# Kernel optimization log

Hardware: AMD Instinct MI355X
Metric: run time of the kernel (lower is better)

The kernel has to match this reference:

```python
import jax, jax.numpy as jnp
import numpy as np

B, S, F, H = 64, 1024, 64, 128


def setup_inputs() -> dict:
    key = jax.random.key(0)
    ks = jax.random.split(key, 12)
    s = 1.0 / np.sqrt(H)
    u = lambda k, shape: jax.random.uniform(k, shape, jnp.float32, -s, s)
    return {
        "x": jax.random.normal(ks[0], (B, S, F), jnp.float32),
        "mu": jax.random.normal(ks[1], (B, 1, F), jnp.float32),
        "W_ih0": u(ks[2], (4 * H, F)),
        "W_hh0": u(ks[3], (4 * H, H)),
        "b_ih0": u(ks[4], (4 * H,)),
        "b_hh0": u(ks[5], (4 * H,)),
        "W_ih1": u(ks[6], (4 * H, H)),
        "W_hh1": u(ks[7], (4 * H, H)),
        "b_ih1": u(ks[8], (4 * H,)),
        "b_hh1": u(ks[9], (4 * H,)),
        "fc_w": u(ks[10], (1, H)),
        "fc_b": u(ks[11], (1,)),
    }


def _cell(x_gates, h, c, Whh, bias):
    # PyTorch LSTM cell: gates ordered i, f, g, o
    g = x_gates + h @ Whh.T + bias
    i, f, gg, o = jnp.split(g, 4, axis=-1)
    c = jax.nn.sigmoid(f) * c + jax.nn.sigmoid(i) * jnp.tanh(gg)
    h = jax.nn.sigmoid(o) * jnp.tanh(c)
    return h, c


def _lstm2(x1, x2, Wih, Whh, bih, bhh):
    # 2-step LSTM layer from zero initial state; returns per-step hidden states
    bias = bih + bhh
    n = x1.shape[0]
    hd = Whh.shape[1]
    h0 = jnp.zeros((n, hd), x1.dtype)
    h1, c1 = _cell(x1 @ Wih.T, h0, h0, Whh, bias)
    h2, _ = _cell(x2 @ Wih.T, h1, c1, Whh, bias)
    return h1, h2


def reference(x, mu, W_ih0, W_hh0, b_ih0, b_hh0, W_ih1, W_hh1, b_ih1, b_hh1, fc_w, fc_b):
    b, s, f = x.shape
    # Every timestep runs an independent 2-step LSTM [x_t, mu] from zero state,
    # so fold (batch, seq) into one big batch of B*S instances.
    x1 = x.reshape(b * s, f)                                   # step-1 inputs
    x2 = jnp.broadcast_to(mu, (b, s, f)).reshape(b * s, f)     # step-2 inputs (mu)
    h1, h2 = _lstm2(x1, x2, W_ih0, W_hh0, b_ih0, b_hh0)        # layer 0
    _, h2 = _lstm2(h1, h2, W_ih1, W_hh1, b_ih1, b_hh1)         # layer 1
    h = jax.nn.relu(h2).reshape(b, s, -1)                      # relu; dropout is identity (eval)
    out = h @ fc_w.T + fc_b                                    # [B, S, 1]
    return out
```

## Files before the change

kernel.cpp:

```cpp
#include <hip/hip_runtime.h>


typedef _Float16 half8 __attribute__((ext_vector_type(8)));
typedef _Float16 half4_t __attribute__((ext_vector_type(4)));
typedef float f32x4 __attribute__((ext_vector_type(4)));

#define L2E  1.4426950408889634f
#define L2E2 2.8853900817779268f

#define WP_WIH0 0
#define WP_WHH0 32768
#define WP_WIH1 98304
#define WP_WHH1 163840
#define WS_BIAS0 458752
#define WS_BIAS1 (458752 + 2048)
#define WS_MUG2  (458752 + 4096)

__global__ void prep_kernel(const float* __restrict__ Wih0,
                            const float* __restrict__ Whh0,
                            const float* __restrict__ Wih1,
                            const float* __restrict__ Whh1,
                            const float* __restrict__ bih0,
                            const float* __restrict__ bhh0,
                            const float* __restrict__ bih1,
                            const float* __restrict__ bhh1,
                            const float* __restrict__ mu,
                            _Float16* __restrict__ Wp,
                            float* __restrict__ bias0f,
                            float* __restrict__ bias1f,
                            float* __restrict__ mu_g2)
{
    int blk = blockIdx.x;
    if (blk >= 113) {
        int o = (blk - 113) * 256 + threadIdx.x;
        int b = o >> 9;
        int n = o & 511;
        float s = bih0[n] + bhh0[n];
        const float* m = mu + b * 64;
        const float* wrow = Wih0 + n * 64;
        #pragma unroll 8
        for (int k = 0; k < 64; ++k) s += m[k] * wrow[k];
        float scale = ((n >> 7) == 2) ? L2E2 : L2E;
        mu_g2[o] = s * scale;
        return;
    }
    if (blk == 112) {
        int i = threadIdx.x;
        float sc_hi = (i < 128) ? L2E2 : L2E;
        bias0f[i]       = (bih0[i]       + bhh0[i])       * L2E;
        bias0f[i + 256] = (bih0[i + 256] + bhh0[i + 256]) * sc_hi;
        bias1f[i]       = (bih1[i]       + bhh1[i])       * L2E;
        bias1f[i + 256] = (bih1[i + 256] + bhh1[i + 256]) * sc_hi;
        return;
    }
    int gidx = blk * 256 + threadIdx.x;
    const float* src; int KC, Kw, local;
    if (gidx < 4096)       { src = Wih0; KC = 2; Kw = 64;  local = gidx; }
    else if (gidx < 12288) { src = Whh0; KC = 4; Kw = 128; local = gidx - 4096; }
    else if (gidx < 20480) { src = Wih1; KC = 4; Kw = 128; local = gidx - 12288; }
    else                   { src = Whh1; KC = 4; Kw = 128; local = gidx - 20480; }
    int lane = local & 63;
    int tmp  = local >> 6;
    int kc   = tmp % KC;
    int nt   = tmp / KC;
    int n  = nt * 16 + (lane & 15);
    int k0 = kc * 32 + (lane >> 4) * 8;
    float scale = ((n >> 7) == 2) ? L2E2 : L2E;
    const float* s = src + n * Kw + k0;
    half8 hv;
    #pragma unroll
    for (int j = 0; j < 8; ++j) hv[j] = (_Float16)(s[j] * scale);
    *(half8*)(Wp + (size_t)gidx * 8) = hv;
}

__device__ __forceinline__ float sig2(float a) {
    return __builtin_amdgcn_rcpf(1.0f + __builtin_amdgcn_exp2f(-a));
}
__device__ __forceinline__ float tanh2(float a) {
    return fmaf(-2.0f, __builtin_amdgcn_rcpf(1.0f + __builtin_amdgcn_exp2f(a)), 1.0f);
}

__device__ __forceinline__ int swz(int row, int col) {
    return (row << 8) + (col ^ ((row & 7) << 4));
}

__device__ __forceinline__ void lds_barrier() {
    asm volatile("s_waitcnt lgkmcnt(0)" ::: "memory");
    __builtin_amdgcn_s_barrier();
    asm volatile("" ::: "memory");
}

template<bool SKIPF>
__device__ __forceinline__ void load_bq(half8 bq[4], const _Float16* __restrict__ Wq,
                                        int KC, int kc, int w, int lane)
{
    #pragma unroll
    for (int g = 0; g < 4; ++g) {
        if (SKIPF && g == 1) continue;
        bq[g] = *(const half8*)(Wq + (((g * 8 + w) * KC + kc) * 64 + lane) * 8);
    }
}

template<int SRC>
__device__ __forceinline__ void load_a(half8 a[4], const char* base, int kc, int c, int q)
{
    #pragma unroll
    for (int mt = 0; mt < 4; ++mt) {
        if (SRC == 0)
            a[mt] = *(const half8*)((const _Float16*)base + (mt * 16 + c) * 72 + kc * 32 + q * 8);
        else
            a[mt] = *(const half8*)(base + swz(mt * 16 + c, kc * 64 + q * 16));
    }
}

template<int KC, int SRC, bool PF, bool FIRST, bool SKIPF, bool NSKIPF>
__device__ __forceinline__ void gemm_pf(const _Float16* __restrict__ Wq,
                                        const char* Abase,
                                        const _Float16* __restrict__ Wnext, int KCnext,
                                        half8 bqc[4], const f32x4 bv[4],
                                        int w, int lane, f32x4 acc[4][4])
{
    const int c = lane & 15, q = lane >> 4;
    #pragma unroll
    for (int kc = 0; kc < KC; ++kc) {
        half8 bqn[4];
        if (kc + 1 < KC)  load_bq<SKIPF>(bqn, Wq, KC, kc + 1, w, lane);
        else if (PF)      load_bq<NSKIPF>(bqn, Wnext, KCnext, 0, w, lane);
        half8 a[4];
        load_a<SRC>(a, Abase, kc, c, q);
        __builtin_amdgcn_s_setprio(1);
        #pragma unroll
        for (int mt = 0; mt < 4; ++mt)
            #pragma unroll
            for (int g = 0; g < 4; ++g) {
                if (SKIPF && g == 1) continue;
                f32x4 cin = (FIRST && kc == 0) ? bv[g] : acc[mt][g];
                acc[mt][g] = __builtin_amdgcn_mfma_f32_16x16x32_f16(bqc[g], a[mt], cin, 0, 0, 0);
            }
        __builtin_amdgcn_s_setprio(0);
        if (kc + 1 < KC) {
            #pragma unroll
            for (int g = 0; g < 4; ++g)
                if (!(SKIPF && g == 1)) bqc[g] = bqn[g];
        } else if (PF) {
            #pragma unroll
            for (int g = 0; g < 4; ++g)
                if (!(NSKIPF && g == 1)) bqc[g] = bqn[g];
        }
    }
}

__global__ __launch_bounds__(512) void lstm_main(
    const float* __restrict__ x, const _Float16* __restrict__ Wp_in,
    const float* __restrict__ bias0f_in, const float* __restrict__ bias1f_in,
    const float* __restrict__ mu_g2_in, const float* __restrict__ fc_w_in,
    const float* __restrict__ fc_b_in, float* __restrict__ out)
{
    __shared__ __align__(16) char smem[49152];
    char* H1s  = smem;
    char* H2s  = smem + 16384;
    char* H11s = smem + 32768;
    _Float16* A0 = (_Float16*)(smem + 16384);

    const int t = threadIdx.x;
    const int w = t >> 6, lane = t & 63, c = lane & 15, q = lane >> 4;
    const int wg = blockIdx.x;
    const int b = wg >> 3;
    const int bq_idx = w * 4 + q;

    half8 bqc[4];
    load_bq<true>(bqc, Wp_in + WP_WIH0, 2, 0, w, lane);

    half8 ax1;
    {
        const float* xp = x + (size_t)wg * 8192 + t * 8;
        float4 u0 = ((const float4*)xp)[0];
        float4 u1 = ((const float4*)xp)[1];
        half8 hv;
        hv[0] = (_Float16)u0.x; hv[1] = (_Float16)u0.y;
        hv[2] = (_Float16)u0.z; hv[3] = (_Float16)u0.w;
        hv[4] = (_Float16)u1.x; hv[5] = (_Float16)u1.y;
        hv[6] = (_Float16)u1.z; hv[7] = (_Float16)u1.w;
        *(half8*)(A0 + (t >> 3) * 72 + (t & 7) * 8) = hv;
        const float* xp1 = x + (size_t)wg * 8192 + 4096 + t * 8;
        float4 v0 = ((const float4*)xp1)[0];
        float4 v1 = ((const float4*)xp1)[1];
        ax1[0] = (_Float16)v0.x; ax1[1] = (_Float16)v0.y;
        ax1[2] = (_Float16)v0.z; ax1[3] = (_Float16)v0.w;
        ax1[4] = (_Float16)v1.x; ax1[5] = (_Float16)v1.y;
        ax1[6] = (_Float16)v1.z; ax1[7] = (_Float16)v1.w;
        if (t < 128) out[(size_t)wg * 128 + t] = fc_b_in[0];
    }
    lds_barrier();

    f32x4 acc[4][4];
    float cc[4][4];

    #pragma unroll
    for (int tile = 0; tile < 2; ++tile) {
        if (tile == 1) lds_barrier();

        {
            f32x4 bv[4];
            {
                const float* bias0f = bias0f_in; asm volatile("" : "+s"(bias0f));
                #pragma unroll
                for (int g = 0; g < 4; ++g)
                    if (g != 1) bv[g] = ((const f32x4*)bias0f)[g * 32 + bq_idx];
            }
            gemm_pf<2, 0, true, true, true, false>(
                Wp_in + WP_WIH0, (const char*)A0,
                Wp_in + WP_WHH0, 4, bqc, bv, w, lane, acc);
        }
        #pragma unroll
        for (int mt = 0; mt < 4; ++mt) {
            half4_t hv;
            #pragma unroll
            for (int r = 0; r < 4; ++r) {
                float c1 = sig2(acc[mt][0][r]) * tanh2(acc[mt][2][r]);
                cc[mt][r] = c1;
                hv[r] = (_Float16)(sig2(acc[mt][3][r]) * tanh2(c1 * L2E2));
            }
            *(half4_t*)(H1s + swz(mt * 16 + c, w * 32 + q * 8)) = hv;
        }
        lds_barrier();

        {
            f32x4 bv[4];
            {
                const float* mu_g2b = mu_g2_in + b * 512; asm volatile("" : "+s"(mu_g2b));
                #pragma unroll
                for (int g = 0; g < 4; ++g)
                    bv[g] = ((const f32x4*)mu_g2b)[g * 32 + bq_idx];
            }
            gemm_pf<4, 1, true, true, false, true>(
                Wp_in + WP_WHH0, H1s,
                Wp_in + WP_WIH1, 4, bqc, bv, w, lane, acc);
        }
        #pragma unroll
        for (int mt = 0; mt < 4; ++mt) {
            half4_t hv;
            #pragma unroll
            for (int r = 0; r < 4; ++r) {
                float c2 = sig2(acc[mt][1][r]) * cc[mt][r]
                         + sig2(acc[mt][0][r]) * tanh2(acc[mt][2][r]);
                hv[r] = (_Float16)(sig2(acc[mt][3][r]) * tanh2(c2 * L2E2));
            }
            *(half4_t*)(H2s + swz(mt * 16 + c, w * 32 + q * 8)) = hv;
        }

        {
            f32x4 bv[4];
            {
                const float* bias1f = bias1f_in; asm volatile("" : "+s"(bias1f));
                #pragma unroll
                for (int g = 0; g < 4; ++g)
                    if (g != 1) bv[g] = ((const f32x4*)bias1f)[g * 32 + bq_idx];
            }
            gemm_pf<4, 1, true, true, true, false>(
                Wp_in + WP_WIH1, H1s,
                Wp_in + WP_WIH1, 4, bqc, bv, w, lane, acc);
        }
        #pragma unroll
        for (int mt = 0; mt < 4; ++mt) {
            half4_t hv;
            #pragma unroll
            for (int r = 0; r < 4; ++r) {
                float c1 = sig2(acc[mt][0][r]) * tanh2(acc[mt][2][r]);
                cc[mt][r] = c1;
                hv[r] = (_Float16)(sig2(acc[mt][3][r]) * tanh2(c1 * L2E2));
            }
            *(half4_t*)(H11s + swz(mt * 16 + c, w * 32 + q * 8)) = hv;
        }
        lds_barrier();

        {
            f32x4 bv[4];
            {
                const float* bias1f = bias1f_in; asm volatile("" : "+s"(bias1f));
                #pragma unroll
                for (int g = 0; g < 4; ++g)
                    bv[g] = ((const f32x4*)bias1f)[g * 32 + bq_idx];
            }
            gemm_pf<4, 1, true, true, false, false>(
                Wp_in + WP_WIH1, H2s,
                Wp_in + WP_WHH1, 4, bqc, bv, w, lane, acc);
        }

        if (tile == 0) {
            lds_barrier();
            *(half8*)(A0 + (t >> 3) * 72 + (t & 7) * 8) = ax1;
            gemm_pf<4, 1, true, false, false, true>(
                Wp_in + WP_WHH1, H11s,
                Wp_in + WP_WIH0, 2, bqc, nullptr, w, lane, acc);
        } else {
            gemm_pf<4, 1, false, false, false, false>(
                Wp_in + WP_WHH1, H11s,
                nullptr, 0, bqc, nullptr, w, lane, acc);
        }

        {
            const float* fc_w = fc_w_in; asm volatile("" : "+s"(fc_w));
            f32x4 fwv = ((const f32x4*)fc_w)[bq_idx];
            #pragma unroll
            for (int mt = 0; mt < 4; ++mt) {
                float v = 0.0f;
                #pragma unroll
                for (int r = 0; r < 4; ++r) {
                    float c2 = sig2(acc[mt][1][r]) * cc[mt][r]
                             + sig2(acc[mt][0][r]) * tanh2(acc[mt][2][r]);
                    float h  = sig2(acc[mt][3][r]) * tanh2(c2 * L2E2);
                    v = fmaf(fmaxf(h, 0.0f), fwv[r], v);
                }
                v += __shfl_xor(v, 16);
                v += __shfl_xor(v, 32);
                if (lane < 16)
                    atomicAdd(out + (size_t)wg * 128 + tile * 64 + mt * 16 + lane, v);
            }
        }
    }
}

extern "C" void kernel_launch(void* const* d_in, const int* in_sizes, int n_in,
                              void* d_out, int out_size, void* d_ws, size_t ws_size,
                              hipStream_t stream)
{
    const float* x    = (const float*)d_in[0];
    const float* mu   = (const float*)d_in[1];
    const float* Wih0 = (const float*)d_in[2];
    const float* Whh0 = (const float*)d_in[3];
    const float* bih0 = (const float*)d_in[4];
    const float* bhh0 = (const float*)d_in[5];
    const float* Wih1 = (const float*)d_in[6];
    const float* Whh1 = (const float*)d_in[7];
    const float* bih1 = (const float*)d_in[8];
    const float* bhh1 = (const float*)d_in[9];
    const float* fcw  = (const float*)d_in[10];
    const float* fcb  = (const float*)d_in[11];
    float* out = (float*)d_out;

    _Float16* Wp  = (_Float16*)d_ws;
    float* bias0f = (float*)((char*)d_ws + WS_BIAS0);
    float* bias1f = (float*)((char*)d_ws + WS_BIAS1);
    float* mu_g2  = (float*)((char*)d_ws + WS_MUG2);

    hipLaunchKernelGGL(prep_kernel, dim3(241), dim3(256), 0, stream,
                       Wih0, Whh0, Wih1, Whh1, bih0, bhh0, bih1, bhh1, mu,
                       Wp, bias0f, bias1f, mu_g2);
    hipLaunchKernelGGL(lstm_main, dim3(512), dim3(512), 0, stream,
                       x, Wp, bias0f, bias1f, mu_g2, fcw, fcb, out);
}
```

Measured before the change: 136.8 us.

## Split each block's two row tiles into separate blocks and fuse sigmoid-tanh products

```diff
diff --git a/kernel.cpp b/kernel.cpp
--- a/kernel.cpp
+++ b/kernel.cpp
@@ -76,8 +76,10 @@
 __device__ __forceinline__ float sig2(float a) {
     return __builtin_amdgcn_rcpf(1.0f + __builtin_amdgcn_exp2f(-a));
 }
-__device__ __forceinline__ float tanh2(float a) {
-    return fmaf(-2.0f, __builtin_amdgcn_rcpf(1.0f + __builtin_amdgcn_exp2f(a)), 1.0f);
+__device__ __forceinline__ float sigtanh(float xs, float yt) {
+    float d = __builtin_amdgcn_exp2f(-xs);
+    float e = __builtin_amdgcn_exp2f(yt);
+    return (e - 1.0f) * __builtin_amdgcn_rcpf((1.0f + d) * (1.0f + e));
 }
 
 __device__ __forceinline__ int swz(int row, int col) {
@@ -165,15 +167,14 @@
     const int t = threadIdx.x;
     const int w = t >> 6, lane = t & 63, c = lane & 15, q = lane >> 4;
     const int wg = blockIdx.x;
-    const int b = wg >> 3;
+    const int b = wg >> 4;
     const int bq_idx = w * 4 + q;
 
     half8 bqc[4];
     load_bq<true>(bqc, Wp_in + WP_WIH0, 2, 0, w, lane);
 
-    half8 ax1;
-    {
-        const float* xp = x + (size_t)wg * 8192 + t * 8;
+    {
+        const float* xp = x + (size_t)wg * 4096 + t * 8;
         float4 u0 = ((const float4*)xp)[0];
         float4 u1 = ((const float4*)xp)[1];
         half8 hv;
@@ -182,141 +183,120 @@
         hv[4] = (_Float16)u1.x; hv[5] = (_Float16)u1.y;
         hv[6] = (_Float16)u1.z; hv[7] = (_Float16)u1.w;
         *(half8*)(A0 + (t >> 3) * 72 + (t & 7) * 8) = hv;
-        const float* xp1 = x + (size_t)wg * 8192 + 4096 + t * 8;
-        float4 v0 = ((const float4*)xp1)[0];
-        float4 v1 = ((const float4*)xp1)[1];
-        ax1[0] = (_Float16)v0.x; ax1[1] = (_Float16)v0.y;
-        ax1[2] = (_Float16)v0.z; ax1[3] = (_Float16)v0.w;
-        ax1[4] = (_Float16)v1.x; ax1[5] = (_Float16)v1.y;
-        ax1[6] = (_Float16)v1.z; ax1[7] = (_Float16)v1.w;
-        if (t < 128) out[(size_t)wg * 128 + t] = fc_b_in[0];
+        if (t < 64) out[(size_t)wg * 64 + t] = fc_b_in[0];
     }
     lds_barrier();
 
     f32x4 acc[4][4];
     float cc[4][4];
 
-    #pragma unroll
-    for (int tile = 0; tile < 2; ++tile) {
-        if (tile == 1) lds_barrier();
-
+    {
+        f32x4 bv[4];
         {
-            f32x4 bv[4];
-            {
-                const float* bias0f = bias0f_in; asm volatile("" : "+s"(bias0f));
-                #pragma unroll
-                for (int g = 0; g < 4; ++g)
-                    if (g != 1) bv[g] = ((const f32x4*)bias0f)[g * 32 + bq_idx];
-            }
-            gemm_pf<2, 0, true, true, true, false>(
-                Wp_in + WP_WIH0, (const char*)A0,
-                Wp_in + WP_WHH0, 4, bqc, bv, w, lane, acc);
-        }
+            const float* bias0f = bias0f_in; asm volatile("" : "+s"(bias0f));
+            #pragma unroll
+            for (int g = 0; g < 4; ++g)
+                if (g != 1) bv[g] = ((const f32x4*)bias0f)[g * 32 + bq_idx];
+        }
+        gemm_pf<2, 0, true, true, true, false>(
+            Wp_in + WP_WIH0, (const char*)A0,
+            Wp_in + WP_WHH0, 4, bqc, bv, w, lane, acc);
+    }
+    #pragma unroll
+    for (int mt = 0; mt < 4; ++mt) {
+        half4_t hv;
+        #pragma unroll
+        for (int r = 0; r < 4; ++r) {
+            float c1 = sigtanh(acc[mt][0][r], acc[mt][2][r]);
+            cc[mt][r] = c1;
+            hv[r] = (_Float16)sigtanh(acc[mt][3][r], c1 * L2E2);
+        }
+        *(half4_t*)(H1s + swz(mt * 16 + c, w * 32 + q * 8)) = hv;
+    }
+    lds_barrier();
+
+    {
+        f32x4 bv[4];
+        {
+            const float* mu_g2b = mu_g2_in + b * 512; asm volatile("" : "+s"(mu_g2b));
+            #pragma unroll
+            for (int g = 0; g < 4; ++g)
+                bv[g] = ((const f32x4*)mu_g2b)[g * 32 + bq_idx];
+        }
+        gemm_pf<4, 1, true, true, false, true>(
+            Wp_in + WP_WHH0, H1s,
+            Wp_in + WP_WIH1, 4, bqc, bv, w, lane, acc);
+    }
+    #pragma unroll
+    for (int mt = 0; mt < 4; ++mt) {
+        half4_t hv;
+        #pragma unroll
+        for (int r = 0; r < 4; ++r) {
+            float c2 = sig2(acc[mt][1][r]) * cc[mt][r]
+                     + sigtanh(acc[mt][0][r], acc[mt][2][r]);
+            hv[r] = (_Float16)sigtanh(acc[mt][3][r], c2 * L2E2);
+        }
+        *(half4_t*)(H2s + swz(mt * 16 + c, w * 32 + q * 8)) = hv;
+    }
+
+    {
+        f32x4 bv[4];
+        {
+            const float* bias1f = bias1f_in; asm volatile("" : "+s"(bias1f));
+            #pragma unroll
+            for (int g = 0; g < 4; ++g)
+                if (g != 1) bv[g] = ((const f32x4*)bias1f)[g * 32 + bq_idx];
+        }
+        gemm_pf<4, 1, true, true, true, false>(
+            Wp_in + WP_WIH1, H1s,
+            Wp_in + WP_WIH1, 4, bqc, bv, w, lane, acc);
+    }
+    #pragma unroll
+    for (int mt = 0; mt < 4; ++mt) {
+        half4_t hv;
+        #pragma unroll
+        for (int r = 0; r < 4; ++r) {
+            float c1 = sigtanh(acc[mt][0][r], acc[mt][2][r]);
+            cc[mt][r] = c1;
+            hv[r] = (_Float16)sigtanh(acc[mt][3][r], c1 * L2E2);
+        }
+        *(half4_t*)(H11s + swz(mt * 16 + c, w * 32 + q * 8)) = hv;
+    }
+    lds_barrier();
+
+    {
+        f32x4 bv[4];
+        {
+            const float* bias1f = bias1f_in; asm volatile("" : "+s"(bias1f));
+            #pragma unroll
+            for (int g = 0; g < 4; ++g)
+                bv[g] = ((const f32x4*)bias1f)[g * 32 + bq_idx];
+        }
+        gemm_pf<4, 1, true, true, false, false>(
+            Wp_in + WP_WIH1, H2s,
+            Wp_in + WP_WHH1, 4, bqc, bv, w, lane, acc);
+    }
+    gemm_pf<4, 1, false, false, false, false>(
+        Wp_in + WP_WHH1, H11s,
+        nullptr, 0, bqc, nullptr, w, lane, acc);
+
+    {
+        const float* fc_w = fc_w_in; asm volatile("" : "+s"(fc_w));
+        f32x4 fwv = ((const f32x4*)fc_w)[bq_idx];
         #pragma unroll
         for (int mt = 0; mt < 4; ++mt) {
-            half4_t hv;
-            #pragma unroll
-            for (int r = 0; r < 4; ++r) {
-                float c1 = sig2(acc[mt][0][r]) * tanh2(acc[mt][2][r]);
-                cc[mt][r] = c1;
-                hv[r] = (_Float16)(sig2(acc[mt][3][r]) * tanh2(c1 * L2E2));
-            }
-            *(half4_t*)(H1s + swz(mt * 16 + c, w * 32 + q * 8)) = hv;
-        }
-        lds_barrier();
-
-        {
-            f32x4 bv[4];
-            {
-                const float* mu_g2b = mu_g2_in + b * 512; asm volatile("" : "+s"(mu_g2b));
-                #pragma unroll
-                for (int g = 0; g < 4; ++g)
-                    bv[g] = ((const f32x4*)mu_g2b)[g * 32 + bq_idx];
-            }
-            gemm_pf<4, 1, true, true, false, true>(
-                Wp_in + WP_WHH0, H1s,
-                Wp_in + WP_WIH1, 4, bqc, bv, w, lane, acc);
-        }
-        #pragma unroll
-        for (int mt = 0; mt < 4; ++mt) {
-            half4_t hv;
+            float v = 0.0f;
             #pragma unroll
             for (int r = 0; r < 4; ++r) {
                 float c2 = sig2(acc[mt][1][r]) * cc[mt][r]
-                         + sig2(acc[mt][0][r]) * tanh2(acc[mt][2][r]);
-                hv[r] = (_Float16)(sig2(acc[mt][3][r]) * tanh2(c2 * L2E2));
+                         + sigtanh(acc[mt][0][r], acc[mt][2][r]);
+                float h  = sigtanh(acc[mt][3][r], c2 * L2E2);
+                v = fmaf(fmaxf(h, 0.0f), fwv[r], v);
             }
-            *(half4_t*)(H2s + swz(mt * 16 + c, w * 32 + q * 8)) = hv;
-        }
-
-        {
-            f32x4 bv[4];
-            {
-                const float* bias1f = bias1f_in; asm volatile("" : "+s"(bias1f));
-                #pragma unroll
-                for (int g = 0; g < 4; ++g)
-                    if (g != 1) bv[g] = ((const f32x4*)bias1f)[g * 32 + bq_idx];
-            }
-            gemm_pf<4, 1, true, true, true, false>(
-                Wp_in + WP_WIH1, H1s,
-                Wp_in + WP_WIH1, 4, bqc, bv, w, lane, acc);
-        }
-        #pragma unroll
-        for (int mt = 0; mt < 4; ++mt) {
-            half4_t hv;
-            #pragma unroll
-            for (int r = 0; r < 4; ++r) {
-                float c1 = sig2(acc[mt][0][r]) * tanh2(acc[mt][2][r]);
-                cc[mt][r] = c1;
-                hv[r] = (_Float16)(sig2(acc[mt][3][r]) * tanh2(c1 * L2E2));
-            }
-            *(half4_t*)(H11s + swz(mt * 16 + c, w * 32 + q * 8)) = hv;
-        }
-        lds_barrier();
-
-        {
-            f32x4 bv[4];
-            {
-                const float* bias1f = bias1f_in; asm volatile("" : "+s"(bias1f));
-                #pragma unroll
-                for (int g = 0; g < 4; ++g)
-                    bv[g] = ((const f32x4*)bias1f)[g * 32 + bq_idx];
-            }
-            gemm_pf<4, 1, true, true, false, false>(
-                Wp_in + WP_WIH1, H2s,
-                Wp_in + WP_WHH1, 4, bqc, bv, w, lane, acc);
-        }
-
-        if (tile == 0) {
-            lds_barrier();
-            *(half8*)(A0 + (t >> 3) * 72 + (t & 7) * 8) = ax1;
-            gemm_pf<4, 1, true, false, false, true>(
-                Wp_in + WP_WHH1, H11s,
-                Wp_in + WP_WIH0, 2, bqc, nullptr, w, lane, acc);
-        } else {
-            gemm_pf<4, 1, false, false, false, false>(
-                Wp_in + WP_WHH1, H11s,
-                nullptr, 0, bqc, nullptr, w, lane, acc);
-        }
-
-        {
-            const float* fc_w = fc_w_in; asm volatile("" : "+s"(fc_w));
-            f32x4 fwv = ((const f32x4*)fc_w)[bq_idx];
-            #pragma unroll
-            for (int mt = 0; mt < 4; ++mt) {
-                float v = 0.0f;
-                #pragma unroll
-                for (int r = 0; r < 4; ++r) {
-                    float c2 = sig2(acc[mt][1][r]) * cc[mt][r]
-                             + sig2(acc[mt][0][r]) * tanh2(acc[mt][2][r]);
-                    float h  = sig2(acc[mt][3][r]) * tanh2(c2 * L2E2);
-                    v = fmaf(fmaxf(h, 0.0f), fwv[r], v);
-                }
-                v += __shfl_xor(v, 16);
-                v += __shfl_xor(v, 32);
-                if (lane < 16)
-                    atomicAdd(out + (size_t)wg * 128 + tile * 64 + mt * 16 + lane, v);
-            }
+            v += __shfl_xor(v, 16);
+            v += __shfl_xor(v, 32);
+            if (lane < 16)
+                atomicAdd(out + (size_t)wg * 64 + mt * 16 + lane, v);
         }
     }
 }
@@ -347,6 +327,6 @@
     hipLaunchKernelGGL(prep_kernel, dim3(241), dim3(256), 0, stream,
                        Wih0, Whh0, Wih1, Whh1, bih0, bhh0, bih1, bhh1, mu,
                        Wp, bias0f, bias1f, mu_g2);
-    hipLaunchKernelGGL(lstm_main, dim3(512), dim3(512), 0, stream,
+    hipLaunchKernelGGL(lstm_main, dim3(1024), dim3(512), 0, stream,
                        x, Wp, bias0f, bias1f, mu_g2, fcw, fcb, out);
 }
```

After: 132.4 us (median of 2 runs). 3.2% less time.
